# Kernel tuning notes

Measured on AMD Instinct MI355X. Metric: run time of the kernel, lower is better.

The kernel has to match this reference:

```python
import jax, jax.numpy as jnp
import numpy as np

EXCHANGE_PERCENT = 0.1  # forward default in the torch source


def _fps_order(pts):
    # pts: [B, N, 3] -> full furthest-point-sampling ordering [B, N] (start at index 0,
    # as torch-points3d's furthest_point_sample does).
    B, N, _ = pts.shape
    mind0 = jnp.full((B, N), jnp.inf, dtype=pts.dtype)
    idx0 = jnp.zeros((B,), dtype=jnp.int32)

    def body(carry, _):
        mind, last = carry
        lp = pts[jnp.arange(B), last]                  # [B, 3] last selected point
        d = jnp.sum((pts - lp[:, None, :]) ** 2, axis=-1)
        mind = jnp.minimum(mind, d)                    # running min-dist to selected set
        nxt = jnp.argmax(mind, axis=1).astype(jnp.int32)
        return (mind, nxt), nxt

    (_, _), rest = jax.lax.scan(body, (mind0, idx0), None, length=N - 1)
    return jnp.concatenate([idx0[:, None], rest.T], axis=1)  # [B, N]


def setup_inputs() -> dict:
    key = jax.random.key(0)
    k1, k2 = jax.random.split(key)
    B, N = 8, 4096
    x = jax.random.normal(k1, (B, N, 3), dtype=jnp.float32)
    curv = jax.random.uniform(k2, (B, N), dtype=jnp.float32)
    return {"x": x, "curv": curv, "k": 16, "num_to_sample": 1024}


def reference(x, curv, k, num_to_sample):
    B, N, _ = x.shape
    S = int(num_to_sample)
    # --- kNN via pairwise (negative squared) distances; xn is computed in the
    # original forward but never used downstream -- reproduced for fidelity. ---
    xx = jnp.sum(x * x, axis=-1)                                     # [B, N]
    pd = 2.0 * jnp.einsum('bnd,bmd->bnm', x, x) - xx[:, :, None] - xx[:, None, :]
    knn_idx = jax.lax.top_k(pd, k)[1]                                # [B, N, k]
    xn = x[jnp.arange(B)[:, None, None], knn_idx]                    # [B, N, k, 3] (unused)
    del xn
    # --- full FPS ordering over all points ---
    idxs = _fps_order(x)                                             # [B, N]
    # --- curvature normalization (note: curv is NOT gathered by idxs before the
    # score product, exactly as in the torch source) ---
    curv_feat = jnp.abs((curv - curv.mean(1, keepdims=True)) / curv.sum(1, keepdims=True))
    curvn = curv - curv.min(1, keepdims=True)
    curvn = curvn / curvn.max(1, keepdims=True)
    curv_feat = jnp.take_along_axis(curv_feat, idxs, axis=1)         # computed, unused (faithful)
    del curv_feat
    scores = jnp.broadcast_to(jnp.linspace(1.0, 0.0, N, dtype=x.dtype)[None], (B, N))
    scores = jnp.take_along_axis(scores, idxs, axis=1)
    sc = scores * curvn                                              # [B, N]
    sca, scb = sc[:, :S], sc[:, S:]
    # bottom_a: descending sort of set A scores
    ba_vals, ba_idx = jax.lax.top_k(sca, S)
    # top_b: ascending sort of set B (topk of negated values)
    nb = N - S
    neg_vals, tb_idx_full = jax.lax.top_k(-scb, nb)
    m = min(S, nb)
    tb_vals = -neg_vals[:, -m:]                                      # largest m of B, ascending
    tb_idx = tb_idx_full[:, -m:] + S                                 # offset into idxs space
    ba_vals_t = ba_vals[:, -m:]
    mask = tb_vals > ba_vals_t
    good_a = jnp.where(~mask, ba_idx[:, -m:], -1)
    good_a = jnp.concatenate([ba_idx[:, :S - m], good_a], axis=-1)   # [B, S]
    good_b = jnp.where(mask, tb_idx, -1)                             # [B, m]
    E = int(EXCHANGE_PERCENT * S)
    final = jnp.concatenate([good_a[:, :S - E], good_b[:, m - E:]], axis=-1)  # [B, S]
    final = jnp.where(final != -1, final, ba_idx)
    # gather actual point indices / coordinates of the selected samples
    pt_idx = jnp.take_along_axis(idxs, final, axis=1)                # [B, S]
    sampled = x[jnp.arange(B)[:, None], pt_idx]                      # [B, S, 3]
    return final, sampled
```

## Files before the change

kernel.cpp:

```cpp
#include <hip/hip_runtime.h>
#include <stdint.h>

typedef unsigned long long u64;
typedef unsigned int u32;

#define BB 8
#define NN 4096
#define SS 1024
#define EE 102
#define NBB 3072
#define FT 256
#define PT 16
#define SEL_T 512

template <int CTRL>
__device__ __forceinline__ float maxdpp(float v) {
  int m = __builtin_amdgcn_update_dpp(0, __float_as_int(v), CTRL, 0xf, 0xf, true);
  return fmaxf(v, __int_as_float(m));
}

__global__ __launch_bounds__(FT) void fps_kernel(const float* __restrict__ x,
                                                 int* __restrict__ idxs) {
  const int b = blockIdx.x;
  const int t = threadIdx.x;
  const int w = t >> 6;
  const int lane = t & 63;
  const float* xb = x + (size_t)b * NN * 3;

  __shared__ float4 lxyz[NN];
  __shared__ u64 rkey[2][4];

  float px[PT], py[PT], pz[PT], mind[PT];

  const float4* xb4 = (const float4*)xb;
  float4 f[12];
#pragma unroll
  for (int j = 0; j < 12; ++j) f[j] = xb4[t * 12 + j];
#pragma unroll
  for (int g = 0; g < 4; ++g) {
    float4 a = f[g * 3 + 0], c = f[g * 3 + 1], d = f[g * 3 + 2];
    px[g * 4 + 0] = a.x; py[g * 4 + 0] = a.y; pz[g * 4 + 0] = a.z;
    px[g * 4 + 1] = a.w; py[g * 4 + 1] = c.x; pz[g * 4 + 1] = c.y;
    px[g * 4 + 2] = c.z; py[g * 4 + 2] = c.w; pz[g * 4 + 2] = d.x;
    px[g * 4 + 3] = d.y; py[g * 4 + 3] = d.z; pz[g * 4 + 3] = d.w;
  }
#pragma unroll
  for (int q = 0; q < PT; ++q) {
    lxyz[t * PT + q] = make_float4(px[q], py[q], pz[q], 0.0f);
    mind[q] = __builtin_inff();
  }
  if (t == 0) idxs[(size_t)b * NN] = 0;
  __syncthreads();

  float4 lp = lxyz[0];
  for (int it = 0; it < NN - 1; ++it) {
    float bestv = -1.0f;
    int bq = 0;
#pragma unroll
    for (int q = 0; q < PT; ++q) {
      float dx = __fsub_rn(px[q], lp.x);
      float dy = __fsub_rn(py[q], lp.y);
      float dz = __fsub_rn(pz[q], lp.z);
      float dd = __fadd_rn(__fadd_rn(__fmul_rn(dx, dx), __fmul_rn(dy, dy)),
                           __fmul_rn(dz, dz));
      float m = fminf(mind[q], dd);
      mind[q] = m;
      if (m > bestv) { bestv = m; bq = q; }
    }
    int besti = t * PT + bq;

    float r = bestv;
    r = maxdpp<0x111>(r);
    r = maxdpp<0x112>(r);
    r = maxdpp<0x114>(r);
    r = maxdpp<0x118>(r);
    r = maxdpp<0x142>(r);
    r = maxdpp<0x143>(r);
    int wmaxb = __builtin_amdgcn_readlane(__float_as_int(r), 63);

    u64 msk = __ballot(__float_as_int(bestv) == wmaxb);
    int flane = __ffsll(msk) - 1;
    int widx = __builtin_amdgcn_readlane(besti, flane);

    u64 key = ((u64)(u32)wmaxb << 32) | (u32)(0xFFFFFFFFu - (u32)widx);
    if (lane == 0) rkey[it & 1][w] = key;
    __syncthreads();

    u64 k0 = rkey[it & 1][0], k1 = rkey[it & 1][1];
    u64 k2 = rkey[it & 1][2], k3 = rkey[it & 1][3];
    u64 m01 = k0 > k1 ? k0 : k1;
    u64 m23 = k2 > k3 ? k2 : k3;
    u64 km = m01 > m23 ? m01 : m23;
    int last = (int)(0xFFFFFFFFu - (u32)(km & 0xFFFFFFFFu));
    if (t == 0) idxs[(size_t)b * NN + it + 1] = last;
    lp = lxyz[last];
  }
}

__global__ __launch_bounds__(SEL_T) void select_kernel(const float* __restrict__ x,
                                                       const float* __restrict__ curv,
                                                       const int* __restrict__ idxs,
                                                       float* __restrict__ out) {
  const int b = blockIdx.x;
  const int t = threadIdx.x;
  __shared__ u64 ka[SS];
  __shared__ u64 kb[4096];
  __shared__ float rmn[8], rmx[8];

  const float* cb = curv + (size_t)b * NN;
  const int* ib = idxs + (size_t)b * NN;

  float mn = __builtin_inff(), mx = -__builtin_inff();
  float cv[8];
#pragma unroll
  for (int q = 0; q < 8; ++q) {
    float v = cb[q * SEL_T + t];
    cv[q] = v;
    mn = fminf(mn, v);
    mx = fmaxf(mx, v);
  }
#pragma unroll
  for (int s = 1; s < 64; s <<= 1) {
    mn = fminf(mn, __shfl_xor(mn, s, 64));
    mx = fmaxf(mx, __shfl_xor(mx, s, 64));
  }
  if ((t & 63) == 0) { rmn[t >> 6] = mn; rmx[t >> 6] = mx; }
  __syncthreads();
  mn = rmn[0]; mx = rmx[0];
#pragma unroll
  for (int w = 1; w < 8; ++w) { mn = fminf(mn, rmn[w]); mx = fmaxf(mx, rmx[w]); }
  float denom = __fsub_rn(mx, mn);

#pragma unroll
  for (int q = 0; q < 8; ++q) {
    int i = q * SEL_T + t;
    float cn = __fdiv_rn(__fsub_rn(cv[q], mn), denom);
    int id = ib[i];
    float sv = __fsub_rn(1.0f, __fdiv_rn((float)id, 4095.0f));
    float scv = __fmul_rn(sv, cn);
    u32 vb = __float_as_uint(scv);
    if (i < SS)
      ka[i] = ((u64)(vb ^ 0xFFFFFFFFu) << 32) | (u32)i;
    else
      kb[i - SS] = ((u64)vb << 32) | (u32)(i - SS);
  }
  for (int i = NBB + t; i < 4096; i += SEL_T) kb[i] = ~0ULL;
  __syncthreads();

  for (u32 k = 2; k <= SS; k <<= 1) {
    for (u32 j = k >> 1; j > 0; j >>= 1) {
      u32 p = (u32)t;
      u32 i = ((p & ~(j - 1)) << 1) | (p & (j - 1));
      u32 l = i | j;
      bool up = ((i & k) == 0);
      u64 a = ka[i], c = ka[l];
      if ((a > c) == up) { ka[i] = c; ka[l] = a; }
      __syncthreads();
    }
  }
  for (u32 k = 2; k <= 4096; k <<= 1) {
    for (u32 j = k >> 1; j > 0; j >>= 1) {
#pragma unroll
      for (u32 p = (u32)t; p < 2048; p += SEL_T) {
        u32 i = ((p & ~(j - 1)) << 1) | (p & (j - 1));
        u32 l = i | j;
        bool up = ((i & k) == 0);
        u64 a = kb[i], c = kb[l];
        if ((a > c) == up) { kb[i] = c; kb[l] = a; }
      }
      __syncthreads();
    }
  }

#pragma unroll
  for (int j0 = 0; j0 < SS; j0 += SEL_T) {
    int j = j0 + t;
    u64 A = ka[j];
    int baid = (int)(u32)(A & 0xFFFFFFFFu);
    u32 babits = ((u32)(A >> 32)) ^ 0xFFFFFFFFu;
    int fin = baid;
    if (j >= SS - EE) {
      u64 Bk = kb[2048 + j];
      u32 tbbits = (u32)(Bk >> 32);
      if (tbbits > babits) fin = (int)(u32)(Bk & 0xFFFFFFFFu) + SS;
    }
    int pt = ib[fin];
    out[(size_t)b * SS + j] = (float)fin;
    const float* xp = x + ((size_t)b * NN + (size_t)pt) * 3;
    float* op = out + (size_t)BB * SS + ((size_t)b * SS + (size_t)j) * 3;
    op[0] = xp[0];
    op[1] = xp[1];
    op[2] = xp[2];
  }
}

extern "C" void kernel_launch(void* const* d_in, const int* in_sizes, int n_in,
                              void* d_out, int out_size, void* d_ws, size_t ws_size,
                              hipStream_t stream) {
  (void)in_sizes; (void)n_in; (void)out_size; (void)ws_size;
  const float* x = (const float*)d_in[0];
  const float* curv = (const float*)d_in[1];
  int* idxs = (int*)d_ws;
  float* out = (float*)d_out;

  fps_kernel<<<BB, FT, 0, stream>>>(x, idxs);
  select_kernel<<<BB, SEL_T, 0, stream>>>(x, curv, idxs, out);
}
```

Before: 2.268 ms.

## Pass winner coordinates through reduction and use packed float2 distance math

The FPS loop no longer reads the selected point's coordinates from a shared-memory point table after the block-wide argmax. Instead, each wave's winning lane selects its candidate's coordinates from registers using a mux tree and publishes them next to the key, and the final reduction picks the coordinates together with the index. This takes a dependent LDS load off the serial critical path of every iteration. The distance computation now uses two-wide float vectors, which can map to packed FP32 instructions, with FP contraction disabled so rounding stays the same. The cost is extra select instructions per iteration and additional shared traffic for the coordinates.

```diff
diff --git a/kernel.cpp b/kernel.cpp
--- a/kernel.cpp
+++ b/kernel.cpp
@@ -1,8 +1,11 @@
 #include <hip/hip_runtime.h>
 #include <stdint.h>
 
+#pragma clang fp contract(off)
+
 typedef unsigned long long u64;
 typedef unsigned int u32;
+typedef float v2f __attribute__((ext_vector_type(2)));
 
 #define BB 8
 #define NN 4096
@@ -11,6 +14,7 @@
 #define NBB 3072
 #define FT 256
 #define PT 16
+#define NP 8
 #define SEL_T 512
 
 template <int CTRL>
@@ -27,10 +31,10 @@
   const int lane = t & 63;
   const float* xb = x + (size_t)b * NN * 3;
 
-  __shared__ float4 lxyz[NN];
   __shared__ u64 rkey[2][4];
-
-  float px[PT], py[PT], pz[PT], mind[PT];
+  __shared__ float4 rcoord[2][4];
+
+  v2f px[NP], py[NP], pz[NP], mind[NP];
 
   const float4* xb4 = (const float4*)xb;
   float4 f[12];
@@ -39,35 +43,41 @@
 #pragma unroll
   for (int g = 0; g < 4; ++g) {
     float4 a = f[g * 3 + 0], c = f[g * 3 + 1], d = f[g * 3 + 2];
-    px[g * 4 + 0] = a.x; py[g * 4 + 0] = a.y; pz[g * 4 + 0] = a.z;
-    px[g * 4 + 1] = a.w; py[g * 4 + 1] = c.x; pz[g * 4 + 1] = c.y;
-    px[g * 4 + 2] = c.z; py[g * 4 + 2] = c.w; pz[g * 4 + 2] = d.x;
-    px[g * 4 + 3] = d.y; py[g * 4 + 3] = d.z; pz[g * 4 + 3] = d.w;
-  }
-#pragma unroll
-  for (int q = 0; q < PT; ++q) {
-    lxyz[t * PT + q] = make_float4(px[q], py[q], pz[q], 0.0f);
-    mind[q] = __builtin_inff();
-  }
-  if (t == 0) idxs[(size_t)b * NN] = 0;
+    px[g * 2 + 0].x = a.x; py[g * 2 + 0].x = a.y; pz[g * 2 + 0].x = a.z;
+    px[g * 2 + 0].y = a.w; py[g * 2 + 0].y = c.x; pz[g * 2 + 0].y = c.y;
+    px[g * 2 + 1].x = c.z; py[g * 2 + 1].x = c.w; pz[g * 2 + 1].x = d.x;
+    px[g * 2 + 1].y = d.y; py[g * 2 + 1].y = d.z; pz[g * 2 + 1].y = d.w;
+  }
+#pragma unroll
+  for (int q = 0; q < NP; ++q) { mind[q].x = __builtin_inff(); mind[q].y = __builtin_inff(); }
+
+  if (t == 0) {
+    idxs[(size_t)b * NN] = 0;
+    rcoord[1][0] = make_float4(px[0].x, py[0].x, pz[0].x, 0.0f);
+  }
   __syncthreads();
-
-  float4 lp = lxyz[0];
+  float4 lp0 = rcoord[1][0];
+  float lx = lp0.x, ly = lp0.y, lz = lp0.z;
+
   for (int it = 0; it < NN - 1; ++it) {
+    const int buf = it & 1;
+    v2f lx2, ly2, lz2;
+    lx2.x = lx; lx2.y = lx; ly2.x = ly; ly2.y = ly; lz2.x = lz; lz2.y = lz;
+
     float bestv = -1.0f;
     int bq = 0;
 #pragma unroll
-    for (int q = 0; q < PT; ++q) {
-      float dx = __fsub_rn(px[q], lp.x);
-      float dy = __fsub_rn(py[q], lp.y);
-      float dz = __fsub_rn(pz[q], lp.z);
-      float dd = __fadd_rn(__fadd_rn(__fmul_rn(dx, dx), __fmul_rn(dy, dy)),
-                           __fmul_rn(dz, dz));
-      float m = fminf(mind[q], dd);
-      mind[q] = m;
-      if (m > bestv) { bestv = m; bq = q; }
-    }
-    int besti = t * PT + bq;
+    for (int q = 0; q < NP; ++q) {
+      v2f dx = px[q] - lx2;
+      v2f dy = py[q] - ly2;
+      v2f dz = pz[q] - lz2;
+      v2f dd = (dx * dx + dy * dy) + dz * dz;
+      float m0 = fminf(mind[q].x, dd.x);
+      float m1 = fminf(mind[q].y, dd.y);
+      mind[q].x = m0; mind[q].y = m1;
+      if (m0 > bestv) { bestv = m0; bq = 2 * q; }
+      if (m1 > bestv) { bestv = m1; bq = 2 * q + 1; }
+    }
 
     float r = bestv;
     r = maxdpp<0x111>(r);
@@ -78,22 +88,57 @@
     r = maxdpp<0x143>(r);
     int wmaxb = __builtin_amdgcn_readlane(__float_as_int(r), 63);
 
+    const bool s0 = (bq & 1) != 0, s1 = (bq & 2) != 0,
+               s2 = (bq & 4) != 0, s3 = (bq & 8) != 0;
+    float e0x[8], e0y[8], e0z[8];
+#pragma unroll
+    for (int j = 0; j < 8; ++j) {
+      e0x[j] = s0 ? px[j].y : px[j].x;
+      e0y[j] = s0 ? py[j].y : py[j].x;
+      e0z[j] = s0 ? pz[j].y : pz[j].x;
+    }
+    float e1x[4], e1y[4], e1z[4];
+#pragma unroll
+    for (int j = 0; j < 4; ++j) {
+      e1x[j] = s1 ? e0x[2 * j + 1] : e0x[2 * j];
+      e1y[j] = s1 ? e0y[2 * j + 1] : e0y[2 * j];
+      e1z[j] = s1 ? e0z[2 * j + 1] : e0z[2 * j];
+    }
+    float e2x[2], e2y[2], e2z[2];
+#pragma unroll
+    for (int j = 0; j < 2; ++j) {
+      e2x[j] = s2 ? e1x[2 * j + 1] : e1x[2 * j];
+      e2y[j] = s2 ? e1y[2 * j + 1] : e1y[2 * j];
+      e2z[j] = s2 ? e1z[2 * j + 1] : e1z[2 * j];
+    }
+    float bx = s3 ? e2x[1] : e2x[0];
+    float by = s3 ? e2y[1] : e2y[0];
+    float bz = s3 ? e2z[1] : e2z[0];
+
     u64 msk = __ballot(__float_as_int(bestv) == wmaxb);
-    int flane = __ffsll(msk) - 1;
-    int widx = __builtin_amdgcn_readlane(besti, flane);
-
-    u64 key = ((u64)(u32)wmaxb << 32) | (u32)(0xFFFFFFFFu - (u32)widx);
-    if (lane == 0) rkey[it & 1][w] = key;
+    int flane = (int)__builtin_ctzll(msk);
+    if (lane == flane) {
+      int besti = t * PT + bq;
+      rkey[buf][w] = ((u64)(u32)wmaxb << 32) | (u32)(0xFFFFFFFFu - (u32)besti);
+      rcoord[buf][w] = make_float4(bx, by, bz, 0.0f);
+    }
     __syncthreads();
 
-    u64 k0 = rkey[it & 1][0], k1 = rkey[it & 1][1];
-    u64 k2 = rkey[it & 1][2], k3 = rkey[it & 1][3];
-    u64 m01 = k0 > k1 ? k0 : k1;
-    u64 m23 = k2 > k3 ? k2 : k3;
-    u64 km = m01 > m23 ? m01 : m23;
+    u64 k0 = rkey[buf][0], k1 = rkey[buf][1];
+    u64 k2 = rkey[buf][2], k3 = rkey[buf][3];
+    float4 q0 = rcoord[buf][0], q1 = rcoord[buf][1];
+    float4 q2 = rcoord[buf][2], q3 = rcoord[buf][3];
+    bool g01 = k0 > k1;
+    u64 ka2 = g01 ? k0 : k1;
+    float ax2 = g01 ? q0.x : q1.x, ay2 = g01 ? q0.y : q1.y, az2 = g01 ? q0.z : q1.z;
+    bool g23 = k2 > k3;
+    u64 kb2 = g23 ? k2 : k3;
+    float bx2 = g23 ? q2.x : q3.x, by2 = g23 ? q2.y : q3.y, bz2 = g23 ? q2.z : q3.z;
+    bool gf = ka2 > kb2;
+    u64 km = gf ? ka2 : kb2;
+    lx = gf ? ax2 : bx2; ly = gf ? ay2 : by2; lz = gf ? az2 : bz2;
     int last = (int)(0xFFFFFFFFu - (u32)(km & 0xFFFFFFFFu));
     if (t == 0) idxs[(size_t)b * NN + it + 1] = last;
-    lp = lxyz[last];
   }
 }
 
```

New measurement: 5.468 ms. +141.1%, slower.
